# Kernel tuning notes

Hardware: AMD Instinct MI355X
Metric: run time of the kernel (lower is better)

## Reference

```python
import jax, jax.numpy as jnp
import numpy as np

KERNEL_SIZE = 4
SCALE = 0.5


def setup_inputs() -> dict:
    key = jax.random.key(0)
    k1, k2, k3 = jax.random.split(key, 3)
    M, K, N = 16384, 1024, 4096
    x = jax.random.normal(k1, (M, K), dtype=jnp.float32)
    weight = jax.random.normal(k2, (N, K), dtype=jnp.float32)
    bias = jax.random.normal(k3, (N,), dtype=jnp.float32)
    return {"x": x, "weight": weight, "bias": bias}


def reference(x, weight, bias):
    # y = x @ W^T + b : (M, N)
    y = jnp.einsum('mk,nk->mn', x, weight) + bias[None, :]
    M, N = y.shape
    valid_n = (N // KERNEL_SIZE) * KERNEL_SIZE
    # MaxPool1d(kernel_size, stride=kernel_size): (M, N//k, k) -> max over window
    pooled = jnp.max(y[:, :valid_n].reshape(M, valid_n // KERNEL_SIZE, KERNEL_SIZE), axis=-1)
    # sum over pooled features, then scale -> (M,)
    return jnp.sum(pooled, axis=-1) * SCALE
```

## Files before the change

kernel.cpp:

```cpp
#include <hip/hip_runtime.h>
#include <stdint.h>

#define M_DIM 16384
#define K_DIM 1024
#define N_DIM 4096
#define BM 128
#define BN 128
#define LDSP 40

#define TILE_ELEMS (128 * K_DIM)
#define CPAD 516

#define GBM 256
#define GBN 256
#define NSLAB 32
#define SLOT_E 16384

typedef __bf16 bf16;
typedef __attribute__((ext_vector_type(8))) __bf16 bf16x8;
typedef __attribute__((ext_vector_type(4))) float f32x4;

__device__ __forceinline__ uint32_t pack2_bf16(float a, float b) {
    uint32_t ua = __float_as_uint(a);
    uint32_t ub = __float_as_uint(b);
    ua += 0x7fffu + ((ua >> 16) & 1u);
    ub += 0x7fffu + ((ub >> 16) & 1u);
    return (ua >> 16) | (ub & 0xffff0000u);
}

__global__ __launch_bounds__(256) void convert_pack_kernel(
    const float* __restrict__ x, const float* __restrict__ w,
    bf16* __restrict__ xp, bf16* __restrict__ wp, float* __restrict__ out)
{
    int g = blockIdx.x;
    const int t = threadIdx.x;
    if (g < (M_DIM / 256)) out[g * 256 + t] = 0.f;

    const float* src;
    bf16* dst;
    if (g < (M_DIM / 16)) {
        src = x + (size_t)g * 16 * K_DIM;  dst = xp;
    } else {
        g -= M_DIM / 16;
        src = w + (size_t)g * 16 * K_DIM;  dst = wp;
    }
    const int tile = g >> 3;
    const int rb   = g & 7;

    __shared__ uint32_t ls[16 * CPAD];

    #pragma unroll
    for (int i = 0; i < 16; ++i) {
        float4 v = ((const float4*)src)[i * 256 + t];
        uint2 d;
        d.x = pack2_bf16(v.x, v.y);
        d.y = pack2_bf16(v.z, v.w);
        *(uint2*)&ls[i * CPAD + t * 2] = d;
    }
    __syncthreads();

    const int wv = t >> 6, l = t & 63;
    const int lrow = l & 15, q = l >> 4;
    uint4* dst4 = (uint4*)(dst + (size_t)tile * TILE_ELEMS);
    #pragma unroll
    for (int it = 0; it < 8; ++it) {
        const int s = wv + it * 4;
        uint4 v = *(const uint4*)&ls[lrow * CPAD + s * 16 + q * 4];
        dst4[(s * 8 + rb) * 64 + l] = v;
    }
}


#define BAR() do { asm volatile("" ::: "memory"); \
                   __builtin_amdgcn_s_barrier();  \
                   asm volatile("" ::: "memory"); } while (0)
#define VMCNT4() asm volatile("s_waitcnt vmcnt(4)" ::: "memory")
#define VMCNT0() asm volatile("s_waitcnt vmcnt(0)" ::: "memory")

#define STG(sl, ch, gsrc) \
    __builtin_amdgcn_global_load_lds( \
        (const __attribute__((address_space(1))) unsigned int*)(gsrc), \
        (__attribute__((address_space(3))) unsigned int*)&sm[(((sl) & 3) * SLOT_E) + (ch) * 4096 + w * 512], \
        16, 0, 0)

#define STG_A(t) do { STG(t, 0, Ag + (size_t)(t) * 4096 + toff); \
                      STG(t, 1, Ag + TILE_ELEMS + (size_t)(t) * 4096 + toff); } while (0)
#define STG_B(t) do { STG(t, 2, Bg + (size_t)(t) * 4096 + toff); \
                      STG(t, 3, Bg + TILE_ELEMS + (size_t)(t) * 4096 + toff); } while (0)

#define RD4(dst, base) do { \
    _Pragma("unroll") \
    for (int _i = 0; _i < 4; ++_i) \
        dst[_i] = *(const bf16x8*)&sm[(base) + _i * 512]; \
} while (0)

#define MFMA16X(Aset, Bset, IB) do { \
    __builtin_amdgcn_s_setprio(1); \
    _Pragma("unroll") \
    for (int ii = 0; ii < 4; ++ii) \
        _Pragma("unroll") \
        for (int jj = 0; jj < 4; ++jj) \
            acc[(IB) + ii][jj] = __builtin_amdgcn_mfma_f32_16x16x32_bf16( \
                Aset[ii], Bset[jj], acc[(IB) + ii][jj], 0, 0, 0); \
    __builtin_amdgcn_s_setprio(0); \
} while (0)

#define SLAB(s, CUR, NXT) do { \
    if ((s) + 2 < NSLAB) STG_A((s) + 2); \
    RD4(Ahi, (((s) & 3) * SLOT_E) + aOff + 2048); \
    MFMA16X(Alo##CUR, Bv##CUR, 0); \
    if ((s) + 2 < NSLAB) STG_B((s) + 2); \
    if ((s) == NSLAB - 2) { VMCNT0(); } else if ((s) < NSLAB - 2) { VMCNT4(); } \
    BAR(); \
    if ((s) + 1 < NSLAB) { \
        RD4(Alo##NXT, ((((s) + 1) & 3) * SLOT_E) + aOff); \
        RD4(Bv##NXT,  ((((s) + 1) & 3) * SLOT_E) + bOff); \
    } \
    MFMA16X(Ahi, Bv##CUR, 4); \
} while (0)

__global__ __launch_bounds__(512, 2) void gemm_pool_ring_kernel(
    const bf16* __restrict__ xp, const bf16* __restrict__ wp,
    const float* __restrict__ bias, float* __restrict__ out)
{
    __shared__ bf16 sm[4 * SLOT_E];

    const int b  = blockIdx.x;
    const int bx = b & (N_DIM / GBN - 1);
    const int by = b >> 4;

    const int tid  = threadIdx.x;
    const int lane = tid & 63;
    const int w    = tid >> 6;
    const int wm   = w >> 2;
    const int wn   = w & 3;
    const int lr   = lane & 15;
    const int quad = lane >> 4;
    const int toff = tid * 8;

    const bf16* __restrict__ Ag = xp + (size_t)(2 * by) * TILE_ELEMS;
    const bf16* __restrict__ Bg = wp + (size_t)(2 * bx) * TILE_ELEMS;

    const int aOff = wm * 4096 + lane * 8;
    const int bOff = 8192 + (wn >> 1) * 4096 + (wn & 1) * 2048 + lane * 8;

    f32x4 acc[8][4] = {};
    bf16x8 AloA[4], AloB[4], Ahi[4], BvA[4], BvB[4];

    STG_A(0); STG_B(0);
    STG_A(1); STG_B(1);
    VMCNT4(); BAR();
    RD4(AloA, aOff);
    RD4(BvA,  bOff);

    #pragma unroll
    for (int sp = 0; sp < NSLAB / 2; ++sp) {
        SLAB(2 * sp,     A, B);
        SLAB(2 * sp + 1, B, A);
    }

    float bv[4];
    #pragma unroll
    for (int j = 0; j < 4; ++j)
        bv[j] = bias[bx * GBN + wn * 64 + j * 16 + lr];

    #pragma unroll
    for (int i = 0; i < 8; ++i) {
        float rs[4] = {0.f, 0.f, 0.f, 0.f};
        #pragma unroll
        for (int j = 0; j < 4; ++j) {
            #pragma unroll
            for (int r = 0; r < 4; ++r) {
                float v = acc[i][j][r] + bv[j];
                v = fmaxf(v, __shfl_xor(v, 1, 64));
                v = fmaxf(v, __shfl_xor(v, 2, 64));
                rs[r] += v;
            }
        }
        #pragma unroll
        for (int r = 0; r < 4; ++r) {
            rs[r] += __shfl_xor(rs[r], 4, 64);
            rs[r] += __shfl_xor(rs[r], 8, 64);
        }
        if (lr == 0) {
            const int row = by * GBM + wm * 128 + i * 16 + quad * 4;
            #pragma unroll
            for (int r = 0; r < 4; ++r)
                atomicAdd(&out[row + r], rs[r] * 0.5f);
        }
    }
}

__global__ __launch_bounds__(256) void fused_linear_pool_kernel(
    const float* __restrict__ x, const float* __restrict__ wt,
    const float* __restrict__ bias, float* __restrict__ out)
{
    __shared__ uint32_t sA[BM * LDSP / 2];
    __shared__ uint32_t sB[BN * LDSP / 2];

    const int tid = threadIdx.x;
    const int bx = blockIdx.x;
    const int by = blockIdx.y;

    const float* Abase = x  + (size_t)by * BM * K_DIM;
    const float* Bbase = wt + (size_t)bx * BN * K_DIM;

    const int lane = tid & 63;
    const int wave = tid >> 6;
    const int wm = wave >> 1;
    const int wn = wave & 1;
    const int lr = lane & 15;
    const int quad = lane >> 4;

    const int srow  = tid >> 2;
    const int scol  = (tid & 3) * 8;
    const int swidx = (tid & 3) * 4;

    f32x4 acc[4][4] = {};

    for (int kt = 0; kt < K_DIM; kt += 32) {
        #pragma unroll
        for (int p = 0; p < 2; ++p) {
            const int r = srow + p * 64;
            const float4* ga = (const float4*)(Abase + (size_t)r * K_DIM + kt + scol);
            const float4* gb = (const float4*)(Bbase + (size_t)r * K_DIM + kt + scol);
            float4 a0 = ga[0], a1 = ga[1], b0 = gb[0], b1 = gb[1];
            uint4 wa;
            wa.x = pack2_bf16(a0.x, a0.y); wa.y = pack2_bf16(a0.z, a0.w);
            wa.z = pack2_bf16(a1.x, a1.y); wa.w = pack2_bf16(a1.z, a1.w);
            *(uint4*)&sA[r * (LDSP / 2) + swidx] = wa;
            uint4 wbv;
            wbv.x = pack2_bf16(b0.x, b0.y); wbv.y = pack2_bf16(b0.z, b0.w);
            wbv.z = pack2_bf16(b1.x, b1.y); wbv.w = pack2_bf16(b1.z, b1.w);
            *(uint4*)&sB[r * (LDSP / 2) + swidx] = wbv;
        }
        __syncthreads();

        bf16x8 af[4], bfr[4];
        #pragma unroll
        for (int i = 0; i < 4; ++i)
            af[i] = *(const bf16x8*)((const bf16*)sA + (wm * 64 + i * 16 + lr) * LDSP + quad * 8);
        #pragma unroll
        for (int j = 0; j < 4; ++j)
            bfr[j] = *(const bf16x8*)((const bf16*)sB + (wn * 64 + j * 16 + lr) * LDSP + quad * 8);

        #pragma unroll
        for (int i = 0; i < 4; ++i)
            #pragma unroll
            for (int j = 0; j < 4; ++j)
                acc[i][j] = __builtin_amdgcn_mfma_f32_16x16x32_bf16(af[i], bfr[j], acc[i][j], 0, 0, 0);
        __syncthreads();
    }

    float bv[4];
    #pragma unroll
    for (int j = 0; j < 4; ++j)
        bv[j] = bias[bx * BN + wn * 64 + j * 16 + lr];

    #pragma unroll
    for (int i = 0; i < 4; ++i) {
        float rsum[4] = {0.f, 0.f, 0.f, 0.f};
        #pragma unroll
        for (int j = 0; j < 4; ++j) {
            #pragma unroll
            for (int r = 0; r < 4; ++r) {
                float t = acc[i][j][r] + bv[j];
                t = fmaxf(t, __shfl_xor(t, 1, 64));
                t = fmaxf(t, __shfl_xor(t, 2, 64));
                t += __shfl_xor(t, 4, 64);
                t += __shfl_xor(t, 8, 64);
                rsum[r] += t;
            }
        }
        if (lr == 0) {
            const int row = by * BM + wm * 64 + i * 16 + quad * 4;
            #pragma unroll
            for (int r = 0; r < 4; ++r)
                atomicAdd(&out[row + r], rsum[r] * 0.5f);
        }
    }
}

extern "C" void kernel_launch(void* const* d_in, const int* in_sizes, int n_in,
                              void* d_out, int out_size, void* d_ws, size_t ws_size,
                              hipStream_t stream) {
    const float* x  = (const float*)d_in[0];
    const float* wt = (const float*)d_in[1];
    const float* bs = (const float*)d_in[2];
    float* out = (float*)d_out;

    const size_t xe = (size_t)M_DIM * K_DIM;
    const size_t we = (size_t)N_DIM * K_DIM;
    const size_t need = (xe + we) * sizeof(bf16);

    if (ws_size >= need) {
        bf16* xp = (bf16*)d_ws;
        bf16* wp = xp + xe;
        const int nconv = (M_DIM / 16) + (N_DIM / 16);
        convert_pack_kernel<<<nconv, 256, 0, stream>>>(x, wt, xp, wp, out);
        gemm_pool_ring_kernel<<<(M_DIM / GBM) * (N_DIM / GBN), 512, 0, stream>>>(xp, wp, bs, out);
    } else {
        hipMemsetAsync(out, 0, (size_t)out_size * sizeof(float), stream);
        dim3 grid(N_DIM / BN, M_DIM / BM);
        fused_linear_pool_kernel<<<grid, 256, 0, stream>>>(x, wt, bs, out);
    }
}
```

Before: 243.7 us.

## Restructure GEMM ring pipeline into two-slab periods with one barrier each

```diff
diff --git a/kernel.cpp b/kernel.cpp
--- a/kernel.cpp
+++ b/kernel.cpp
@@ -74,8 +74,8 @@
 #define BAR() do { asm volatile("" ::: "memory"); \
                    __builtin_amdgcn_s_barrier();  \
                    asm volatile("" ::: "memory"); } while (0)
-#define VMCNT4() asm volatile("s_waitcnt vmcnt(4)" ::: "memory")
 #define VMCNT0() asm volatile("s_waitcnt vmcnt(0)" ::: "memory")
+#define LGKM0()  asm volatile("s_waitcnt lgkmcnt(0)" ::: "memory")
 
 #define STG(sl, ch, gsrc) \
     __builtin_amdgcn_global_load_lds( \
@@ -87,6 +87,8 @@
                       STG(t, 1, Ag + TILE_ELEMS + (size_t)(t) * 4096 + toff); } while (0)
 #define STG_B(t) do { STG(t, 2, Bg + (size_t)(t) * 4096 + toff); \
                       STG(t, 3, Bg + TILE_ELEMS + (size_t)(t) * 4096 + toff); } while (0)
+
+#define SLB(s) (((s) & 3) * SLOT_E)
 
 #define RD4(dst, base) do { \
     _Pragma("unroll") \
@@ -105,21 +107,25 @@
     __builtin_amdgcn_s_setprio(0); \
 } while (0)
 
-#define SLAB(s, CUR, NXT) do { \
-    if ((s) + 2 < NSLAB) STG_A((s) + 2); \
-    RD4(Ahi, (((s) & 3) * SLOT_E) + aOff + 2048); \
-    MFMA16X(Alo##CUR, Bv##CUR, 0); \
-    if ((s) + 2 < NSLAB) STG_B((s) + 2); \
-    if ((s) == NSLAB - 2) { VMCNT0(); } else if ((s) < NSLAB - 2) { VMCNT4(); } \
+#define PERIOD(u, v) do { \
+    if ((u) + 2 < NSLAB) { STG_A((u) + 2); STG_B((u) + 2); \
+                           STG_A((v) + 2); STG_B((v) + 2); } \
+    RD4(AloA, SLB(u) + aOff); \
+    RD4(BvA,  SLB(u) + bOff); \
+    MFMA16X(AloA, BvA, 0); \
+    RD4(Ahi,  SLB(u) + aOff + 2048); \
+    RD4(AloB, SLB(v) + aOff); \
+    RD4(BvB,  SLB(v) + bOff); \
+    MFMA16X(Ahi, BvA, 4); \
+    MFMA16X(AloB, BvB, 0); \
+    RD4(Ahi,  SLB(v) + aOff + 2048); \
+    MFMA16X(Ahi, BvB, 4); \
+    LGKM0(); \
+    VMCNT0(); \
     BAR(); \
-    if ((s) + 1 < NSLAB) { \
-        RD4(Alo##NXT, ((((s) + 1) & 3) * SLOT_E) + aOff); \
-        RD4(Bv##NXT,  ((((s) + 1) & 3) * SLOT_E) + bOff); \
-    } \
-    MFMA16X(Ahi, Bv##CUR, 4); \
 } while (0)
 
-__global__ __launch_bounds__(512, 2) void gemm_pool_ring_kernel(
+__global__ __launch_bounds__(512, 2) void gemm_pool_ring2_kernel(
     const bf16* __restrict__ xp, const bf16* __restrict__ wp,
     const float* __restrict__ bias, float* __restrict__ out)
 {
@@ -149,14 +155,11 @@
 
     STG_A(0); STG_B(0);
     STG_A(1); STG_B(1);
-    VMCNT4(); BAR();
-    RD4(AloA, aOff);
-    RD4(BvA,  bOff);
+    VMCNT0(); BAR();
 
     #pragma unroll
     for (int sp = 0; sp < NSLAB / 2; ++sp) {
-        SLAB(2 * sp,     A, B);
-        SLAB(2 * sp + 1, B, A);
+        PERIOD(2 * sp, 2 * sp + 1);
     }
 
     float bv[4];
@@ -298,7 +301,7 @@
         bf16* wp = xp + xe;
         const int nconv = (M_DIM / 16) + (N_DIM / 16);
         convert_pack_kernel<<<nconv, 256, 0, stream>>>(x, wt, xp, wp, out);
-        gemm_pool_ring_kernel<<<(M_DIM / GBM) * (N_DIM / GBN), 512, 0, stream>>>(xp, wp, bs, out);
+        gemm_pool_ring2_kernel<<<(M_DIM / GBM) * (N_DIM / GBN), 512, 0, stream>>>(xp, wp, bs, out);
     } else {
         hipMemsetAsync(out, 0, (size_t)out_size * sizeof(float), stream);
         dim3 grid(N_DIM / BN, M_DIM / BM);
```

Result: no change. 248.4 us (+1.9%).
